# Optimization experiments

Measured on AMD Instinct MI355X. Metric: run time of the kernel, lower is better.

The kernel has to match this reference:

```python
import jax, jax.numpy as jnp
import numpy as np

COST_CLASS = 1.0
COST_BBOX = 5.0
COST_GIOU = 2.0
EPS = 1e-7


def box_cxcywh_to_xyxy(x):
    cx, cy, w, h = x[..., 0], x[..., 1], x[..., 2], x[..., 3]
    return jnp.stack([cx - 0.5 * w, cy - 0.5 * h, cx + 0.5 * w, cy + 0.5 * h], axis=-1)


def generalized_box_iou(boxes1, boxes2):
    # boxes1: [N,4] xyxy, boxes2: [M,4] xyxy -> [N,M]
    area1 = (boxes1[:, 2] - boxes1[:, 0]) * (boxes1[:, 3] - boxes1[:, 1])
    area2 = (boxes2[:, 2] - boxes2[:, 0]) * (boxes2[:, 3] - boxes2[:, 1])
    lt = jnp.maximum(boxes1[:, None, :2], boxes2[None, :, :2])
    rb = jnp.minimum(boxes1[:, None, 2:], boxes2[None, :, 2:])
    wh = jnp.clip(rb - lt, 0.0)
    inter = wh[..., 0] * wh[..., 1]
    union = area1[:, None] + area2[None, :] - inter
    iou = inter / (union + EPS)
    # smallest enclosing box
    lt_c = jnp.minimum(boxes1[:, None, :2], boxes2[None, :, :2])
    rb_c = jnp.maximum(boxes1[:, None, 2:], boxes2[None, :, 2:])
    wh_c = jnp.clip(rb_c - lt_c, 0.0)
    c_area = wh_c[..., 0] * wh_c[..., 1]
    return iou - (c_area - union) / (c_area + EPS)


def setup_inputs() -> dict:
    key = jax.random.key(0)
    k1, k2, k3, k4 = jax.random.split(key, 4)
    bs, nq, nc, nt = 16, 900, 256, 800
    pred_logits = jax.random.normal(k1, (bs, nq, nc), dtype=jnp.float32)
    pred_boxes = jax.random.uniform(k2, (bs, nq, 4), dtype=jnp.float32)
    tgt_labels = jax.random.randint(k3, (nt,), 0, nc, dtype=jnp.int64)
    tgt_boxes = jax.random.uniform(k4, (nt, 4), dtype=jnp.float32)
    return {"pred_logits": pred_logits, "pred_boxes": pred_boxes,
            "tgt_labels": tgt_labels, "tgt_boxes": tgt_boxes}


def reference(pred_logits, pred_boxes, tgt_labels, tgt_boxes):
    # Returns the full pairwise matching cost tensor C: [bs, num_queries, total_targets].
    # (The scipy linear_sum_assignment / CPU Hungarian step consumes this on host.)
    bs, nq, nc = pred_logits.shape
    out_prob = jax.nn.softmax(pred_logits.reshape(bs * nq, nc), axis=-1)  # [N, nc]
    out_bbox = pred_boxes.reshape(bs * nq, 4)                              # [N, 4]
    cost_class = -out_prob[:, tgt_labels]                                  # [N, M]
    cost_bbox = jnp.abs(out_bbox[:, None, :] - tgt_boxes[None, :, :]).sum(-1)  # L1 cdist [N, M]
    cost_giou = -generalized_box_iou(box_cxcywh_to_xyxy(out_bbox),
                                     box_cxcywh_to_xyxy(tgt_boxes))        # [N, M]
    C = COST_BBOX * cost_bbox + COST_CLASS * cost_class + COST_GIOU * cost_giou
    return C.reshape(bs, nq, -1)
```

## Files before the change

kernel.cpp:

```cpp
#include <hip/hip_runtime.h>
#include <hip/hip_bf16.h>


constexpr float EPS = 1e-7f;

__global__ __launch_bounds__(256) void matcher_kernel(
    const float* __restrict__ logits,
    const float* __restrict__ pboxes,
    const int*   __restrict__ labels,
    const float* __restrict__ tboxes,
    float* __restrict__ out,
    int N, int M, int lbl_mask)
{
    const int wave = threadIdx.x >> 6;
    const int lane = threadIdx.x & 63;
    const int n    = blockIdx.x * 4 + wave;

    __shared__ float s_prob[4][256];

    if (n < N) {
        const float4 lg =
            reinterpret_cast<const float4*>(logits)[(size_t)n * 64 + lane];

        float mx = fmaxf(fmaxf(lg.x, lg.y), fmaxf(lg.z, lg.w));
        #pragma unroll
        for (int off = 32; off > 0; off >>= 1)
            mx = fmaxf(mx, __shfl_xor(mx, off, 64));

        const float e0 = __expf(lg.x - mx);
        const float e1 = __expf(lg.y - mx);
        const float e2 = __expf(lg.z - mx);
        const float e3 = __expf(lg.w - mx);

        float s = (e0 + e1) + (e2 + e3);
        #pragma unroll
        for (int off = 32; off > 0; off >>= 1)
            s += __shfl_xor(s, off, 64);

        const float inv = __builtin_amdgcn_rcpf(s);
        reinterpret_cast<float4*>(&s_prob[wave][0])[lane] =
            make_float4(e0 * inv, e1 * inv, e2 * inv, e3 * inv);
    }
    __syncthreads();
    if (n >= N) return;

    const float4 pb = reinterpret_cast<const float4*>(pboxes)[n];
    const float ax1 = pb.x - 0.5f * pb.z, ay1 = pb.y - 0.5f * pb.w;
    const float ax2 = pb.x + 0.5f * pb.z, ay2 = pb.y + 0.5f * pb.w;
    const float area1 = (ax2 - ax1) * (ay2 - ay1);

    const float* sp   = s_prob[wave];
    float*       orow = out + (size_t)n * M;
    const int items = M >> 2;

    for (int item = lane; item < items; item += 64) {
        const int4 lb = reinterpret_cast<const int4*>(labels)[item];
        const float4* tbp = reinterpret_cast<const float4*>(tboxes) + item * 4;
        const int ls[4] = {lb.x, lb.y, lb.z, lb.w};
        float res[4];
        #pragma unroll
        for (int j = 0; j < 4; ++j) {
            const float4 tb  = tbp[j];
            const float prob = sp[ls[j] & lbl_mask];

            const float l1 = fabsf(pb.x - tb.x) + fabsf(pb.y - tb.y)
                           + fabsf(pb.z - tb.z) + fabsf(pb.w - tb.w);

            const float bx1 = tb.x - 0.5f * tb.z, by1 = tb.y - 0.5f * tb.w;
            const float bx2 = tb.x + 0.5f * tb.z, by2 = tb.y + 0.5f * tb.w;
            const float area2 = tb.z * tb.w;

            const float iw = fmaxf(fminf(ax2, bx2) - fmaxf(ax1, bx1), 0.0f);
            const float ih = fmaxf(fminf(ay2, by2) - fmaxf(ay1, by1), 0.0f);
            const float inter = iw * ih;
            const float uni   = area1 + area2 - inter;
            const float iou   = inter * __builtin_amdgcn_rcpf(uni + EPS);

            const float cw = fmaxf(ax2, bx2) - fminf(ax1, bx1);
            const float ch = fmaxf(ay2, by2) - fminf(ay1, by1);
            const float carea = cw * ch;

            const float giou =
                iou - (carea - uni) * __builtin_amdgcn_rcpf(carea + EPS);
            res[j] = 5.0f * l1 - prob - 2.0f * giou;
        }
        reinterpret_cast<float4*>(orow)[item] =
            make_float4(res[0], res[1], res[2], res[3]);
    }

    for (int m = (items << 2) + lane; m < M; m += 64) {
        const float4 tb  = reinterpret_cast<const float4*>(tboxes)[m];
        const float prob = sp[labels[m] & lbl_mask];
        const float l1 = fabsf(pb.x - tb.x) + fabsf(pb.y - tb.y)
                       + fabsf(pb.z - tb.z) + fabsf(pb.w - tb.w);
        const float bx1 = tb.x - 0.5f * tb.z, by1 = tb.y - 0.5f * tb.w;
        const float bx2 = tb.x + 0.5f * tb.z, by2 = tb.y + 0.5f * tb.w;
        const float area2 = tb.z * tb.w;
        const float iw = fmaxf(fminf(ax2, bx2) - fmaxf(ax1, bx1), 0.0f);
        const float ih = fmaxf(fminf(ay2, by2) - fmaxf(ay1, by1), 0.0f);
        const float inter = iw * ih;
        const float uni   = area1 + area2 - inter;
        const float iou   = inter * __builtin_amdgcn_rcpf(uni + EPS);
        const float cw = fmaxf(ax2, bx2) - fminf(ax1, bx1);
        const float ch = fmaxf(ay2, by2) - fminf(ay1, by1);
        const float carea = cw * ch;
        const float giou =
            iou - (carea - uni) * __builtin_amdgcn_rcpf(carea + EPS);
        orow[m] = 5.0f * l1 - prob - 2.0f * giou;
    }
}

extern "C" void kernel_launch(void* const* d_in, const int* in_sizes, int n_in,
                              void* d_out, int out_size, void* d_ws, size_t ws_size,
                              hipStream_t stream) {
    const float* logits = (const float*)d_in[0];
    const float* pboxes = (const float*)d_in[1];
    const int*   labels = (const int*)d_in[2];
    const float* tboxes = (const float*)d_in[3];

    const int N  = in_sizes[1] / 4;
    const int M  = in_sizes[2];
    const int NC = in_sizes[0] / N;
    const int lbl_mask = NC - 1;

    const int grid = (N + 3) / 4;
    matcher_kernel<<<grid, 256, 0, stream>>>(
        logits, pboxes, labels, tboxes, (float*)d_out, N, M, lbl_mask);
}
```

Measured before the change: 96.50 us.

## Cache target boxes and labels in registers, process four queries per wave

Adds a specialised kernel for NC=256 and M=800. It stages target boxes and labels in LDS once per block and keeps them in registers. Each wave then handles four query rows in turn, so target loads are reused across 16 queries per block. This trades higher register pressure and a shape-specialised path for fewer global and L2 reads of the target data and fewer block launches. A generic fallback kernel is kept for other shapes.

```diff
diff --git a/kernel.cpp b/kernel.cpp
--- a/kernel.cpp
+++ b/kernel.cpp
@@ -4,42 +4,139 @@
 
 constexpr float EPS = 1e-7f;
 
-__global__ __launch_bounds__(256) void matcher_kernel(
+__device__ __forceinline__ float pair_cost(
+    const float4& pb, float ax1, float ay1, float ax2, float ay2, float area1,
+    const float4& tb, float prob)
+{
+    const float l1 = fabsf(pb.x - tb.x) + fabsf(pb.y - tb.y)
+                   + fabsf(pb.z - tb.z) + fabsf(pb.w - tb.w);
+
+    const float bx1 = tb.x - 0.5f * tb.z, by1 = tb.y - 0.5f * tb.w;
+    const float bx2 = tb.x + 0.5f * tb.z, by2 = tb.y + 0.5f * tb.w;
+    const float area2 = tb.z * tb.w;
+
+    const float iw = fmaxf(fminf(ax2, bx2) - fmaxf(ax1, bx1), 0.0f);
+    const float ih = fmaxf(fminf(ay2, by2) - fmaxf(ay1, by1), 0.0f);
+    const float inter = iw * ih;
+    const float uni   = area1 + area2 - inter;
+    const float iou   = inter * __builtin_amdgcn_rcpf(uni + EPS);
+
+    const float cw = fmaxf(ax2, bx2) - fminf(ax1, bx1);
+    const float ch = fmaxf(ay2, by2) - fminf(ay1, by1);
+    const float carea = cw * ch;
+
+    const float giou = iou - (carea - uni) * __builtin_amdgcn_rcpf(carea + EPS);
+    return 5.0f * l1 - prob - 2.0f * giou;
+}
+
+__global__ __launch_bounds__(256) void matcher_opt(
     const float* __restrict__ logits,
     const float* __restrict__ pboxes,
     const int*   __restrict__ labels,
     const float* __restrict__ tboxes,
     float* __restrict__ out,
-    int N, int M, int lbl_mask)
+    int N)
+{
+    const int wave = threadIdx.x >> 6;
+    const int lane = threadIdx.x & 63;
+
+    __shared__ float4 s_tb[800];
+    __shared__ int    s_lb[800];
+    __shared__ float  s_prob[4][256];
+
+    for (int i = threadIdx.x; i < 800; i += 256) {
+        s_tb[i] = reinterpret_cast<const float4*>(tboxes)[i];
+        s_lb[i] = labels[i] & 255;
+    }
+    __syncthreads();
+
+    float4 tb[3][4];
+    int    po[3][4];
+    #pragma unroll
+    for (int g = 0; g < 3; ++g) {
+        const int m0 = (g * 64 + lane) * 4;
+        #pragma unroll
+        for (int j = 0; j < 4; ++j) {
+            tb[g][j] = s_tb[m0 + j];
+            po[g][j] = s_lb[m0 + j];
+        }
+    }
+    float4 tbt = make_float4(0.f, 0.f, 0.f, 0.f);
+    int pot = 0;
+    if (lane < 32) { tbt = s_tb[768 + lane]; pot = s_lb[768 + lane]; }
+
+    float* sp = s_prob[wave];
+
+    const int n0 = (blockIdx.x * 4 + wave) * 4;
+    #pragma unroll 1
+    for (int r = 0; r < 4; ++r) {
+        const int n = n0 + r;
+        if (n >= N) return;
+
+        const float4 lg =
+            reinterpret_cast<const float4*>(logits)[(size_t)n * 64 + lane];
+        float mx = fmaxf(fmaxf(lg.x, lg.y), fmaxf(lg.z, lg.w));
+        #pragma unroll
+        for (int off = 32; off > 0; off >>= 1)
+            mx = fmaxf(mx, __shfl_xor(mx, off, 64));
+        const float e0 = __expf(lg.x - mx), e1 = __expf(lg.y - mx);
+        const float e2 = __expf(lg.z - mx), e3 = __expf(lg.w - mx);
+        float s = (e0 + e1) + (e2 + e3);
+        #pragma unroll
+        for (int off = 32; off > 0; off >>= 1)
+            s += __shfl_xor(s, off, 64);
+        const float inv = __builtin_amdgcn_rcpf(s);
+        reinterpret_cast<float4*>(sp)[lane] =
+            make_float4(e0 * inv, e1 * inv, e2 * inv, e3 * inv);
+
+        const float4 pb = reinterpret_cast<const float4*>(pboxes)[n];
+        const float ax1 = pb.x - 0.5f * pb.z, ay1 = pb.y - 0.5f * pb.w;
+        const float ax2 = pb.x + 0.5f * pb.z, ay2 = pb.y + 0.5f * pb.w;
+        const float area1 = pb.z * pb.w;
+
+        float* orow = out + (size_t)n * 800;
+
+        #pragma unroll
+        for (int g = 0; g < 3; ++g) {
+            float4 res;
+            res.x = pair_cost(pb, ax1, ay1, ax2, ay2, area1, tb[g][0], sp[po[g][0]]);
+            res.y = pair_cost(pb, ax1, ay1, ax2, ay2, area1, tb[g][1], sp[po[g][1]]);
+            res.z = pair_cost(pb, ax1, ay1, ax2, ay2, area1, tb[g][2], sp[po[g][2]]);
+            res.w = pair_cost(pb, ax1, ay1, ax2, ay2, area1, tb[g][3], sp[po[g][3]]);
+            reinterpret_cast<float4*>(orow)[g * 64 + lane] = res;
+        }
+        if (lane < 32)
+            orow[768 + lane] =
+                pair_cost(pb, ax1, ay1, ax2, ay2, area1, tbt, sp[pot]);
+    }
+}
+
+__global__ __launch_bounds__(256) void matcher_generic(
+    const float* __restrict__ logits, const float* __restrict__ pboxes,
+    const int* __restrict__ labels, const float* __restrict__ tboxes,
+    float* __restrict__ out, int N, int M, int NC, int lbl_mask)
 {
     const int wave = threadIdx.x >> 6;
     const int lane = threadIdx.x & 63;
     const int n    = blockIdx.x * 4 + wave;
 
-    __shared__ float s_prob[4][256];
+    extern __shared__ float s_dyn[];
+    float* sp = s_dyn + wave * NC;
 
     if (n < N) {
-        const float4 lg =
-            reinterpret_cast<const float4*>(logits)[(size_t)n * 64 + lane];
-
-        float mx = fmaxf(fmaxf(lg.x, lg.y), fmaxf(lg.z, lg.w));
+        float mx = -3.4e38f;
+        for (int c = lane; c < NC; c += 64) mx = fmaxf(mx, logits[(size_t)n * NC + c]);
         #pragma unroll
-        for (int off = 32; off > 0; off >>= 1)
-            mx = fmaxf(mx, __shfl_xor(mx, off, 64));
-
-        const float e0 = __expf(lg.x - mx);
-        const float e1 = __expf(lg.y - mx);
-        const float e2 = __expf(lg.z - mx);
-        const float e3 = __expf(lg.w - mx);
-
-        float s = (e0 + e1) + (e2 + e3);
+        for (int off = 32; off > 0; off >>= 1) mx = fmaxf(mx, __shfl_xor(mx, off, 64));
+        float s = 0.f;
+        for (int c = lane; c < NC; c += 64) {
+            const float e = __expf(logits[(size_t)n * NC + c] - mx);
+            sp[c] = e; s += e;
+        }
         #pragma unroll
-        for (int off = 32; off > 0; off >>= 1)
-            s += __shfl_xor(s, off, 64);
-
+        for (int off = 32; off > 0; off >>= 1) s += __shfl_xor(s, off, 64);
         const float inv = __builtin_amdgcn_rcpf(s);
-        reinterpret_cast<float4*>(&s_prob[wave][0])[lane] =
-            make_float4(e0 * inv, e1 * inv, e2 * inv, e3 * inv);
+        for (int c = lane; c < NC; c += 64) sp[c] *= inv;
     }
     __syncthreads();
     if (n >= N) return;
@@ -47,66 +144,13 @@
     const float4 pb = reinterpret_cast<const float4*>(pboxes)[n];
     const float ax1 = pb.x - 0.5f * pb.z, ay1 = pb.y - 0.5f * pb.w;
     const float ax2 = pb.x + 0.5f * pb.z, ay2 = pb.y + 0.5f * pb.w;
-    const float area1 = (ax2 - ax1) * (ay2 - ay1);
+    const float area1 = pb.z * pb.w;
+    float* orow = out + (size_t)n * M;
 
-    const float* sp   = s_prob[wave];
-    float*       orow = out + (size_t)n * M;
-    const int items = M >> 2;
-
-    for (int item = lane; item < items; item += 64) {
-        const int4 lb = reinterpret_cast<const int4*>(labels)[item];
-        const float4* tbp = reinterpret_cast<const float4*>(tboxes) + item * 4;
-        const int ls[4] = {lb.x, lb.y, lb.z, lb.w};
-        float res[4];
-        #pragma unroll
-        for (int j = 0; j < 4; ++j) {
-            const float4 tb  = tbp[j];
-            const float prob = sp[ls[j] & lbl_mask];
-
-            const float l1 = fabsf(pb.x - tb.x) + fabsf(pb.y - tb.y)
-                           + fabsf(pb.z - tb.z) + fabsf(pb.w - tb.w);
-
-            const float bx1 = tb.x - 0.5f * tb.z, by1 = tb.y - 0.5f * tb.w;
-            const float bx2 = tb.x + 0.5f * tb.z, by2 = tb.y + 0.5f * tb.w;
-            const float area2 = tb.z * tb.w;
-
-            const float iw = fmaxf(fminf(ax2, bx2) - fmaxf(ax1, bx1), 0.0f);
-            const float ih = fmaxf(fminf(ay2, by2) - fmaxf(ay1, by1), 0.0f);
-            const float inter = iw * ih;
-            const float uni   = area1 + area2 - inter;
-            const float iou   = inter * __builtin_amdgcn_rcpf(uni + EPS);
-
-            const float cw = fmaxf(ax2, bx2) - fminf(ax1, bx1);
-            const float ch = fmaxf(ay2, by2) - fminf(ay1, by1);
-            const float carea = cw * ch;
-
-            const float giou =
-                iou - (carea - uni) * __builtin_amdgcn_rcpf(carea + EPS);
-            res[j] = 5.0f * l1 - prob - 2.0f * giou;
-        }
-        reinterpret_cast<float4*>(orow)[item] =
-            make_float4(res[0], res[1], res[2], res[3]);
-    }
-
-    for (int m = (items << 2) + lane; m < M; m += 64) {
-        const float4 tb  = reinterpret_cast<const float4*>(tboxes)[m];
-        const float prob = sp[labels[m] & lbl_mask];
-        const float l1 = fabsf(pb.x - tb.x) + fabsf(pb.y - tb.y)
-                       + fabsf(pb.z - tb.z) + fabsf(pb.w - tb.w);
-        const float bx1 = tb.x - 0.5f * tb.z, by1 = tb.y - 0.5f * tb.w;
-        const float bx2 = tb.x + 0.5f * tb.z, by2 = tb.y + 0.5f * tb.w;
-        const float area2 = tb.z * tb.w;
-        const float iw = fmaxf(fminf(ax2, bx2) - fmaxf(ax1, bx1), 0.0f);
-        const float ih = fmaxf(fminf(ay2, by2) - fmaxf(ay1, by1), 0.0f);
-        const float inter = iw * ih;
-        const float uni   = area1 + area2 - inter;
-        const float iou   = inter * __builtin_amdgcn_rcpf(uni + EPS);
-        const float cw = fmaxf(ax2, bx2) - fminf(ax1, bx1);
-        const float ch = fmaxf(ay2, by2) - fminf(ay1, by1);
-        const float carea = cw * ch;
-        const float giou =
-            iou - (carea - uni) * __builtin_amdgcn_rcpf(carea + EPS);
-        orow[m] = 5.0f * l1 - prob - 2.0f * giou;
+    for (int m = lane; m < M; m += 64) {
+        const float4 tb = reinterpret_cast<const float4*>(tboxes)[m];
+        orow[m] = pair_cost(pb, ax1, ay1, ax2, ay2, area1, tb,
+                            sp[labels[m] & lbl_mask]);
     }
 }
 
@@ -121,9 +165,17 @@
     const int N  = in_sizes[1] / 4;
     const int M  = in_sizes[2];
     const int NC = in_sizes[0] / N;
-    const int lbl_mask = NC - 1;
 
-    const int grid = (N + 3) / 4;
-    matcher_kernel<<<grid, 256, 0, stream>>>(
-        logits, pboxes, labels, tboxes, (float*)d_out, N, M, lbl_mask);
+    if (NC == 256 && M == 800) {
+        const int waves = (N + 3) / 4;
+        const int grid  = (waves + 3) / 4;
+        matcher_opt<<<grid, 256, 0, stream>>>(
+            logits, pboxes, labels, tboxes, (float*)d_out, N);
+    } else {
+        int lbl_mask = 1; while (lbl_mask < NC) lbl_mask <<= 1;
+        --lbl_mask;
+        const int grid = (N + 3) / 4;
+        matcher_generic<<<grid, 256, 4 * NC * sizeof(float), stream>>>(
+            logits, pboxes, labels, tboxes, (float*)d_out, N, M, NC, lbl_mask);
+    }
 }
```

Result: no change. 95.82 us (-0.7%).
